# Kernel optimization log

Measured on AMD Instinct MI355X. Metric: run time of the kernel, lower is better.

The kernel has to match this reference:

```python
import jax, jax.numpy as jnp
import numpy as np

VOCAB = 32000
DIM = 1024
DEPTH = 4
SEQ = 512
HEADS = 16
NMB = 4
MAXMEM = NMB * SEQ  # 2048
RAMP = 128
COEF = 1e-06
B = 4
DH = DIM // HEADS


def _ln(x, g, b):
    mu = jnp.mean(x, axis=-1, keepdims=True)
    v = jnp.mean((x - mu) ** 2, axis=-1, keepdims=True)
    return (x - mu) / jnp.sqrt(v + 1e-5) * g + b


def setup_inputs() -> dict:
    key = jax.random.key(0)
    ks = jax.random.split(key, 24)
    s = 0.02
    inp = {
        'tokens': jax.random.randint(ks[0], (B, SEQ), 0, VOCAB),
        'mems': jax.random.normal(ks[1], (DEPTH, B, MAXMEM, DIM), jnp.float32) * s,
        'times': jax.random.randint(ks[2], (DEPTH, MAXMEM), 0, 4096, dtype=jnp.int32),
        'token_emb': jax.random.normal(ks[3], (VOCAB, DIM), jnp.float32) * s,
        'expire_W': jax.random.normal(ks[4], (DEPTH, DIM), jnp.float32) * s,
        'expire_b': jnp.full((DEPTH,), -float(MAXMEM), jnp.float32),  # torch init constant
        'ln1_g': jnp.ones((DEPTH, DIM), jnp.float32),
        'ln1_b': jnp.zeros((DEPTH, DIM), jnp.float32),
        'Wq': jax.random.normal(ks[5], (DEPTH, DIM, DIM), jnp.float32) * s,
        'Wkv': jax.random.normal(ks[6], (DEPTH, DIM, 2 * DIM), jnp.float32) * s,
        'Wo': jax.random.normal(ks[7], (DEPTH, DIM, DIM), jnp.float32) * s,
        'bo': jnp.zeros((DEPTH, DIM), jnp.float32),
        'ln2_g': jnp.ones((DEPTH, DIM), jnp.float32),
        'ln2_b': jnp.zeros((DEPTH, DIM), jnp.float32),
        'W1': jax.random.normal(ks[8], (DEPTH, DIM, 4 * DIM), jnp.float32) * s,
        'b1': jnp.zeros((DEPTH, 4 * DIM), jnp.float32),
        'W2': jax.random.normal(ks[9], (DEPTH, 4 * DIM, DIM), jnp.float32) * s,
        'b2': jnp.zeros((DEPTH, DIM), jnp.float32),
        'logits_W': jax.random.normal(ks[10], (DIM, VOCAB), jnp.float32) * s,
        'logits_b': jnp.zeros((VOCAB,), jnp.float32),
    }
    return inp


def reference(tokens, mems, times, token_emb, expire_W, expire_b, ln1_g, ln1_b,
              Wq, Wkv, Wo, bo, ln2_g, ln2_b, W1, b1, W2, b2, logits_W, logits_b):
    n, M = SEQ, MAXMEM
    scale = DH ** -0.5
    x = token_emb[tokens]  # (B, n, DIM)
    # causal mask over concat(mem, x): query i may attend key j iff j <= i + M
    causal = jnp.triu(jnp.ones((n, M + n), bool), k=M + 1)  # True = masked
    aux = jnp.float32(0.0)
    new_mems, new_times = [], []
    tnew = jnp.arange(n - 1, -1, -1, dtype=times.dtype)
    for d in range(DEPTH):
        mem = mems[d]                       # (B, M, DIM)
        t = times[d].astype(jnp.float32)    # (M,)
        hidden = x
        # --- expire span: per-memory-slot soft retention mask ---
        exps = jax.nn.sigmoid(mem @ expire_W[d] + expire_b[d]) * M  # (B, M)
        r = exps[:, None, None, :] - t[None, None, None, :]          # (B,1,1,M)
        r = jnp.pad(r, ((0, 0), (0, 0), (0, 0), (0, n)), constant_values=1.0)
        emask = jnp.clip(r / RAMP + 1.0, 0.0, 1.0)                   # (B,1,1,M+n)
        # --- pre-norm causal attention over concat(mem, x_normed) ---
        xn = _ln(x, ln1_g[d], ln1_b[d])
        q = (xn @ Wq[d]).reshape(B, n, HEADS, DH).transpose(0, 2, 1, 3)
        ctx = jnp.concatenate([mem, xn], axis=1)                     # (B, M+n, DIM)
        kv = ctx @ Wkv[d]
        k = kv[..., :DIM].reshape(B, M + n, HEADS, DH).transpose(0, 2, 1, 3)
        v = kv[..., DIM:].reshape(B, M + n, HEADS, DH).transpose(0, 2, 1, 3)
        dots = jnp.einsum('bhid,bhjd->bhij', q, k) * scale
        dots = jnp.where(causal, -jnp.inf, dots)
        attn = jax.nn.softmax(dots, axis=-1) * emask
        out = jnp.einsum('bhij,bhjd->bhid', attn, v)
        out = out.transpose(0, 2, 1, 3).reshape(B, n, DIM)
        x = out @ Wo[d] + bo[d] + x
        # --- pre-norm FFN ---
        xn2 = _ln(x, ln2_g[d], ln2_b[d])
        x = jax.nn.gelu(xn2 @ W1[d] + b1[d], approximate=False) @ W2[d] + b2[d] + x
        aux = aux + (exps / SEQ).sum() * COEF
        # --- memory bookkeeping (detached) ---
        new_mems.append(jax.lax.stop_gradient(
            jnp.concatenate([mem, hidden], axis=1)[:, -M:]))
        new_times.append(jnp.concatenate([times[d] + n, tnew])[-M:])
    logits = x @ logits_W + logits_b
    return (logits, jnp.stack(new_mems), jnp.stack(new_times), aux)
```

## Files before the change

### kernel.cpp

```cpp
#include <hip/hip_runtime.h>
#include <cmath>

#define DIMC   1024
#define SEQC   512
#define BC     4
#define MC     2048
#define CTXC   2560
#define HEADSC 16
#define DHC    64
#define VOCABC 32000

using short8 = __attribute__((ext_vector_type(8))) short;
using f32x4  = __attribute__((ext_vector_type(4))) float;
using u16x4  = __attribute__((ext_vector_type(4))) unsigned short;
using u16x8  = __attribute__((ext_vector_type(8))) unsigned short;

__device__ __forceinline__ unsigned short f2bf(float f) {
    unsigned u = __float_as_uint(f);
    unsigned r = (u + 0x7fffu + ((u >> 16) & 1u)) >> 16;
    return (unsigned short)r;
}

__device__ __forceinline__ void glds16(const unsigned short* g, char* l) {
    __builtin_amdgcn_global_load_lds(
        (const __attribute__((address_space(1))) void*)g,
        (__attribute__((address_space(3))) void*)l, 16, 0, 0);
}

__global__ __launch_bounds__(256) void embed_kernel(const int* __restrict__ tokens,
                                                    const float* __restrict__ emb,
                                                    float* __restrict__ x) {
    int row = blockIdx.x;
    int tok = tokens[row];
    const float4 v = *(const float4*)(emb + (size_t)tok * DIMC + threadIdx.x * 4);
    *(float4*)(x + (size_t)row * DIMC + threadIdx.x * 4) = v;
}

__global__ __launch_bounds__(256) void times_init_kernel(const int* __restrict__ times,
                                                         float* __restrict__ out_times,
                                                         float* __restrict__ aux) {
    int i = blockIdx.x * 256 + threadIdx.x;
    if (i == 0) aux[0] = 0.0f;
    if (i < 4 * MC) {
        int d = i >> 11, m = i & (MC - 1);
        out_times[i] = (m < MC - SEQC) ? (float)(times[d * MC + SEQC + m] + SEQC)
                                       : (float)(MC - 1 - m);
    }
}

#define PREP_MEM 8192
#define PREP_XC  10240
#define PREP_LN  12288
#define PREP_TOT 24576
__global__ __launch_bounds__(256) void prep_kernel(
    const float* __restrict__ mem_d, const float* __restrict__ x,
    const float* __restrict__ eW, const float* __restrict__ eb,
    float* __restrict__ exps, float* __restrict__ aux,
    unsigned short* __restrict__ mem_b, float* __restrict__ out_mems_d,
    const float* __restrict__ g1, const float* __restrict__ b1v,
    unsigned short* __restrict__ xn_b,
    const float* __restrict__ Wq, const float* __restrict__ Wkv,
    const float* __restrict__ Wo, const float* __restrict__ W1,
    const float* __restrict__ W2,
    unsigned short* __restrict__ wq_t, unsigned short* __restrict__ wkv_t,
    unsigned short* __restrict__ wo_t, unsigned short* __restrict__ w1_t,
    unsigned short* __restrict__ w2_t) {
    __shared__ float sh[1056];
    const int bid = blockIdx.x, tid = threadIdx.x;
    if (bid < PREP_MEM) {
        int row = bid;
        int m = row & 2047, b = row >> 11;
        const float4 v = *(const float4*)(mem_d + (size_t)row * DIMC + tid * 4);
        const float4 w = *(const float4*)(eW + tid * 4);
        float s = v.x * w.x + v.y * w.y + v.z * w.z + v.w * w.w;
        for (int off = 32; off; off >>= 1) s += __shfl_down(s, off, 64);
        int wid = tid >> 6, lane = tid & 63;
        if (lane == 0) sh[wid] = s;
        u16x4 o = { f2bf(v.x), f2bf(v.y), f2bf(v.z), f2bf(v.w) };
        *(u16x4*)(mem_b + (size_t)row * DIMC + tid * 4) = o;
        if (m >= SEQC)
            *(float4*)(out_mems_d + ((size_t)(b * MC + m - SEQC)) * DIMC + tid * 4) = v;
        __syncthreads();
        if (tid == 0) {
            float z = sh[0] + sh[1] + sh[2] + sh[3] + eb[0];
            float e = (float)MC / (1.0f + expf(-z));
            exps[row] = e;
            atomicAdd(aux, e * (1e-6f / (float)SEQC));
        }
    } else if (bid < PREP_XC) {
        int r = bid - PREP_MEM;
        int b = r >> 9, i = r & 511;
        const float4 v = *(const float4*)(x + (size_t)r * DIMC + tid * 4);
        *(float4*)(out_mems_d + ((size_t)(b * MC + MC - SEQC + i)) * DIMC + tid * 4) = v;
    } else if (bid < PREP_LN) {
        int row = bid - PREP_XC;
        const float4 v = *(const float4*)(x + (size_t)row * DIMC + tid * 4);
        float s = v.x + v.y + v.z + v.w;
        float q = v.x * v.x + v.y * v.y + v.z * v.z + v.w * v.w;
        for (int off = 32; off; off >>= 1) {
            s += __shfl_down(s, off, 64);
            q += __shfl_down(q, off, 64);
        }
        int wid = tid >> 6, lane = tid & 63;
        if (lane == 0) { sh[wid] = s; sh[4 + wid] = q; }
        __syncthreads();
        if (tid == 0) {
            float S = sh[0] + sh[1] + sh[2] + sh[3];
            float Q = sh[4] + sh[5] + sh[6] + sh[7];
            float mu = S / DIMC;
            float var = Q / DIMC - mu * mu;
            sh[8] = mu;
            sh[9] = rsqrtf(var + 1e-5f);
        }
        __syncthreads();
        float mu = sh[8], rstd = sh[9];
        const float4 gg = *(const float4*)(g1 + tid * 4);
        const float4 bb = *(const float4*)(b1v + tid * 4);
        u16x4 o = { f2bf((v.x - mu) * rstd * gg.x + bb.x),
                    f2bf((v.y - mu) * rstd * gg.y + bb.y),
                    f2bf((v.z - mu) * rstd * gg.z + bb.z),
                    f2bf((v.w - mu) * rstd * gg.w + bb.w) };
        *(u16x4*)(xn_b + (size_t)row * DIMC + tid * 4) = o;
    } else {
        int t = bid - PREP_LN;
        const float* W; unsigned short* Wt; int K, N, tx, ty;
        if (t < 1024)      { W = Wq;  Wt = wq_t;  K = 1024; N = 1024; tx = t & 31;  ty = t >> 5; }
        else if (t < 3072) { int u = t - 1024; W = Wkv; Wt = wkv_t; K = 1024; N = 2048; tx = u & 63;  ty = u >> 6; }
        else if (t < 4096) { int u = t - 3072; W = Wo;  Wt = wo_t;  K = 1024; N = 1024; tx = u & 31;  ty = u >> 5; }
        else if (t < 8192) { int u = t - 4096; W = W1;  Wt = w1_t;  K = 1024; N = 4096; tx = u & 127; ty = u >> 7; }
        else               { int u = t - 8192; W = W2;  Wt = w2_t;  K = 4096; N = 1024; tx = u & 31;  ty = u >> 5; }
        int n0 = tx * 32, k0 = ty * 32;
        int r = tid >> 3, c = (tid & 7) * 4;
        const float4 v = *(const float4*)(W + (size_t)(k0 + r) * N + n0 + c);
        sh[r * 33 + c] = v.x; sh[r * 33 + c + 1] = v.y;
        sh[r * 33 + c + 2] = v.z; sh[r * 33 + c + 3] = v.w;
        __syncthreads();
        u16x4 o = { f2bf(sh[(c + 0) * 33 + r]), f2bf(sh[(c + 1) * 33 + r]),
                    f2bf(sh[(c + 2) * 33 + r]), f2bf(sh[(c + 3) * 33 + r]) };
        *(u16x4*)(Wt + (size_t)(n0 + r) * K + k0 + c) = o;
    }
}

__global__ __launch_bounds__(64) void compact_kernel(
    const float* __restrict__ exps, const int* __restrict__ times_d,
    int* __restrict__ cidx, float* __restrict__ em_c, int* __restrict__ cnt) {
    int b = blockIdx.x, lane = threadIdx.x;
    int c = 0;
    for (int it = 0; it < 32; ++it) {
        int j = it * 64 + lane;
        float e = exps[b * MC + j];
        float rr = (e - (float)times_d[j]) * (1.0f / 128.0f) + 1.0f;
        float em = fminf(fmaxf(rr, 0.0f), 1.0f);
        unsigned long long mk = __ballot(em > 0.0f);
        int pos = c + __popcll(mk & ((1ull << lane) - 1ull));
        if (em > 0.0f) {
            cidx[b * 2048 + pos] = j;
            em_c[b * 2048 + pos] = em;
        }
        c += __popcll(mk);
    }
    int padded = (c + 63) & ~63;
    for (int p = c + lane; p < padded; p += 64) {
        cidx[b * 2048 + p] = 0;
        em_c[b * 2048 + p] = 0.0f;
    }
    if (lane == 0) cnt[b] = padded >> 6;
}

__global__ __launch_bounds__(256) void ln_kernel(const float* __restrict__ in,
                                                 const float* __restrict__ g,
                                                 const float* __restrict__ b,
                                                 unsigned short* __restrict__ outb) {
    int row = blockIdx.x;
    int tid = threadIdx.x;
    const float4 v = *(const float4*)(in + (size_t)row * DIMC + tid * 4);
    float s = v.x + v.y + v.z + v.w;
    float q = v.x * v.x + v.y * v.y + v.z * v.z + v.w * v.w;
    for (int off = 32; off; off >>= 1) {
        s += __shfl_down(s, off, 64);
        q += __shfl_down(q, off, 64);
    }
    __shared__ float ss[4], sq[4];
    int wid = tid >> 6, lane = tid & 63;
    if (lane == 0) { ss[wid] = s; sq[wid] = q; }
    __syncthreads();
    if (tid == 0) {
        float S = ss[0] + ss[1] + ss[2] + ss[3];
        float Q = sq[0] + sq[1] + sq[2] + sq[3];
        float mu = S / DIMC;
        float var = Q / DIMC - mu * mu;
        ss[0] = mu;
        sq[0] = rsqrtf(var + 1e-5f);
    }
    __syncthreads();
    float mu = ss[0], rstd = sq[0];
    const float4 gg = *(const float4*)(g + tid * 4);
    const float4 bb = *(const float4*)(b + tid * 4);
    u16x4 o = { f2bf((v.x - mu) * rstd * gg.x + bb.x),
                f2bf((v.y - mu) * rstd * gg.y + bb.y),
                f2bf((v.z - mu) * rstd * gg.z + bb.z),
                f2bf((v.w - mu) * rstd * gg.w + bb.w) };
    *(u16x4*)(outb + (size_t)row * DIMC + tid * 4) = o;
}

__global__ __launch_bounds__(256) void wt_kernel(const float* __restrict__ W,
                                                 unsigned short* __restrict__ Wt,
                                                 int K, int N) {
    __shared__ float t[32][33];
    int tid = threadIdx.x;
    int n0 = blockIdx.x * 32, k0 = blockIdx.y * 32;
    int r = tid >> 3, c = (tid & 7) * 4;
    const float4 v = *(const float4*)(W + (size_t)(k0 + r) * N + n0 + c);
    t[r][c] = v.x; t[r][c + 1] = v.y; t[r][c + 2] = v.z; t[r][c + 3] = v.w;
    __syncthreads();
    u16x4 o = { f2bf(t[c + 0][r]), f2bf(t[c + 1][r]),
                f2bf(t[c + 2][r]), f2bf(t[c + 3][r]) };
    *(u16x4*)(Wt + (size_t)(n0 + r) * K + k0 + c) = o;
}

__global__ __launch_bounds__(256) void vt_kernel(const unsigned short* __restrict__ kvb,
                                                 unsigned short* __restrict__ vT) {
    __shared__ unsigned short t[64][72];
    int jt = blockIdx.x, dt = blockIdx.y, b = blockIdx.z;
    int j0 = MC + jt * 64;
    int tid = threadIdx.x;
    int r = tid >> 3, c = (tid & 7) * 8;
    #pragma unroll
    for (int p = 0; p < 2; ++p) {
        u16x8 v = *(const u16x8*)(kvb + ((size_t)(b * CTXC + j0 + r + p * 32)) * 2048
                                  + 1024 + dt * 64 + c);
        *(u16x8*)&t[r + p * 32][c] = v;
    }
    __syncthreads();
    #pragma unroll
    for (int p = 0; p < 2; ++p) {
        int dr = r + p * 32;
        u16x8 o = { t[c + 0][dr], t[c + 1][dr], t[c + 2][dr], t[c + 3][dr],
                    t[c + 4][dr], t[c + 5][dr], t[c + 6][dr], t[c + 7][dr] };
        *(u16x8*)(vT + ((size_t)(b * 1024 + dt * 64 + dr)) * CTXC + j0 + c) = o;
    }
}

__global__ __launch_bounds__(256) void vtc_kernel(const unsigned short* __restrict__ kvb,
                                                  const int* __restrict__ cidx,
                                                  const int* __restrict__ cnt,
                                                  unsigned short* __restrict__ vTc) {
    int ct = blockIdx.x, dt = blockIdx.y, b = blockIdx.z;
    if (ct >= cnt[b]) return;
    __shared__ unsigned short t[64][72];
    int tid = threadIdx.x;
    int r = tid >> 3, c = (tid & 7) * 8;
    #pragma unroll
    for (int p = 0; p < 2; ++p) {
        int row = cidx[b * 2048 + ct * 64 + r + p * 32];
        u16x8 v = *(const u16x8*)(kvb + ((size_t)(b * CTXC + row)) * 2048
                                  + 1024 + dt * 64 + c);
        *(u16x8*)&t[r + p * 32][c] = v;
    }
    __syncthreads();
    #pragma unroll
    for (int p = 0; p < 2; ++p) {
        int dr = r + p * 32;
        u16x8 o = { t[c + 0][dr], t[c + 1][dr], t[c + 2][dr], t[c + 3][dr],
                    t[c + 4][dr], t[c + 5][dr], t[c + 6][dr], t[c + 7][dr] };
        *(u16x8*)(vTc + ((size_t)(b * 1024 + dt * 64 + dr)) * 2048 + ct * 64 + c) = o;
    }
}

template<bool GATHER, bool BIAS, bool GELU, bool RES, int RT>
__device__ __forceinline__ void gemm_body(
    unsigned short* As, unsigned short* Bs,
    const unsigned short* __restrict__ A, const unsigned short* __restrict__ A2,
    const unsigned short* __restrict__ Wt, const float* __restrict__ bias,
    const float* __restrict__ res, float* __restrict__ Cf,
    unsigned short* __restrict__ Cb, int K, int N, int bx, int by) {
    constexpr int MF = RT / 32;
    const int tid = threadIdx.x;
    const int lane = tid & 63, wave = tid >> 6;
    const int row0 = by * RT, col0 = bx * 128;

    const int seg = tid & 3;
    const int rr0 = tid >> 2;
    const unsigned short* arow[RT / 64];
    #pragma unroll
    for (int p = 0; p < RT / 64; ++p) {
        int r = row0 + p * 64 + rr0;
        if (GATHER) {
            int b = r / CTXC, rm = r - b * CTXC;
            arow[p] = (rm < MC) ? A + ((size_t)(b * MC + rm)) * K
                                : A2 + ((size_t)(b * SEQC + rm - MC)) * K;
        } else {
            arow[p] = A + (size_t)r * K;
        }
        arow[p] += seg * 8;
    }
    const unsigned short* brow[2];
    #pragma unroll
    for (int p = 0; p < 2; ++p)
        brow[p] = Wt + (size_t)(col0 + p * 64 + rr0) * K + seg * 8;

    char* lA0 = (char*)As + (size_t)(tid & 192) * 16;
    char* lB0 = (char*)Bs + (size_t)(tid & 192) * 16;
    char* lB1 = lB0 + 4096;

    f32x4 acc[MF][4] = {};

    const int wr = (wave >> 1) * (RT / 2), wc = (wave & 1) * 64;
    const int fr = lane & 15;
    const int k8 = (lane >> 4) * 8;
    const unsigned short* Ar = As + (size_t)(wr + fr) * 32 + k8;
    const unsigned short* Br = Bs + (size_t)(wc + fr) * 32 + k8;

    for (int k0 = 0; k0 < K; k0 += 32) {
        glds16(arow[0] + k0, lA0);
        if (RT == 128) glds16(arow[1] + k0, lA0 + 4096);
        glds16(brow[0] + k0, lB0);
        glds16(brow[1] + k0, lB1);
        __syncthreads();
        short8 a[MF], b[4];
        #pragma unroll
        for (int m = 0; m < MF; ++m) a[m] = *(const short8*)(Ar + m * 16 * 32);
        #pragma unroll
        for (int n = 0; n < 4; ++n) b[n] = *(const short8*)(Br + n * 16 * 32);
        #pragma unroll
        for (int m = 0; m < MF; ++m)
            #pragma unroll
            for (int n = 0; n < 4; ++n)
                acc[m][n] = __builtin_amdgcn_mfma_f32_16x16x32_bf16(a[m], b[n], acc[m][n], 0, 0, 0);
        __syncthreads();
    }

    const int orow = row0 + wr + (lane >> 4) * 4;
    const int ocol = col0 + wc + fr;
    #pragma unroll
    for (int n = 0; n < 4; ++n) {
        int c = ocol + n * 16;
        float bv = BIAS ? bias[c] : 0.0f;
        #pragma unroll
        for (int m = 0; m < MF; ++m) {
            #pragma unroll
            for (int i = 0; i < 4; ++i) {
                size_t idx = (size_t)(orow + m * 16 + i) * N + c;
                float v = acc[m][n][i] + bv;
                if (GELU) v = 0.5f * v * (1.0f + erff(v * 0.70710678118f));
                if (RES) v += res[idx];
                if (Cf) Cf[idx] = v;
                if (Cb) Cb[idx] = f2bf(v);
            }
        }
    }
}

__global__ __launch_bounds__(256) void qkv_gemm_kernel(
    const unsigned short* __restrict__ xn_b, const unsigned short* __restrict__ mem_b,
    const unsigned short* __restrict__ wq_t, const unsigned short* __restrict__ wkv_t,
    unsigned short* __restrict__ qb, unsigned short* __restrict__ kvb) {
    __shared__ unsigned short As[128 * 32];
    __shared__ unsigned short Bs[128 * 32];
    int id = blockIdx.x;
    if (id < 128) {
        gemm_body<false, false, false, false, 128>(As, Bs, xn_b, nullptr, wq_t,
            nullptr, nullptr, nullptr, qb, 1024, 1024, id & 7, id >> 3);
    } else {
        id -= 128;
        gemm_body<true, false, false, false, 128>(As, Bs, mem_b, xn_b, wkv_t,
            nullptr, nullptr, nullptr, kvb, 1024, 2048, id & 15, id >> 4);
    }
}

__global__ __launch_bounds__(256) void gemm64_kernel(
    const unsigned short* __restrict__ A, const unsigned short* __restrict__ Wt,
    const float* __restrict__ bias, const float* __restrict__ res,
    float* __restrict__ Cf, unsigned short* __restrict__ Cb, int K) {
    __shared__ unsigned short As[64 * 32];
    __shared__ unsigned short Bs[128 * 32];
    gemm_body<false, true, false, true, 64>(As, Bs, A, nullptr, Wt, bias, res,
        Cf, Cb, K, 1024, blockIdx.x, blockIdx.y);
}

__global__ __launch_bounds__(256) void ffn1_kernel(
    const unsigned short* __restrict__ A, const unsigned short* __restrict__ Wt,
    const float* __restrict__ bias, unsigned short* __restrict__ Cb) {
    __shared__ unsigned short As[128 * 32];
    __shared__ unsigned short Bs[128 * 32];
    gemm_body<false, true, true, false, 128>(As, Bs, A, nullptr, Wt, bias, nullptr,
        nullptr, Cb, 1024, 4096, blockIdx.x, blockIdx.y);
}

__global__ __launch_bounds__(256) void logits_kernel(
    const unsigned short* __restrict__ A, const unsigned short* __restrict__ Wt,
    const float* __restrict__ bias, float* __restrict__ Cf) {
    __shared__ unsigned short As[128 * 32];
    __shared__ unsigned short Bs[128 * 32];
    gemm_body<false, true, false, false, 128>(As, Bs, A, nullptr, Wt, bias, nullptr,
        Cf, nullptr, 1024, VOCABC, blockIdx.y, blockIdx.x);
}

__global__ __launch_bounds__(256) void attn_mfma_kernel(
    const unsigned short* __restrict__ qb,
    const unsigned short* __restrict__ kvb,
    const unsigned short* __restrict__ vT,
    const unsigned short* __restrict__ vTc,
    const int* __restrict__ cidx,
    const float* __restrict__ em_c,
    const int* __restrict__ cnt,
    unsigned short* __restrict__ outb) {
    __shared__ unsigned short K_s[64 * 64];
    __shared__ unsigned short V_s[64 * 64];
    __shared__ unsigned short p_s[4][16][72];
    __shared__ float em_s[64];
    const int tid = threadIdx.x;
    const int lane = tid & 63, wave = tid >> 6;
    const int qt = blockIdx.x, h = blockIdx.y, b = blockIdx.z;
    const int fr = lane & 15, g = lane >> 4;
    const int gq = qt * 64 + wave * 16;

    short8 aq[2];
    {
        const unsigned short* qp = qb + ((size_t)(b * SEQC + gq + fr)) * DIMC + h * DHC + g * 8;
        aq[0] = *(const short8*)qp;
        aq[1] = *(const short8*)(qp + 32);
    }

    const int sr = tid >> 3, ss = tid & 7;
    char* ldk = (char*)K_s + (tid & 192) * 16;
    char* ldv = (char*)V_s + (tid & 192) * 16;

    f32x4 acc_o[4] = {};
    float m_q = -1e30f, l_q = 0.0f;

    for (int kt = 0; kt < 32; ++kt) {
        const int jbase = kt * 64;
        __syncthreads();
        #pragma unroll
        for (int p = 0; p < 2; ++p) {
            int r = sr + p * 32, sw = (ss ^ (r & 7)) * 8;
            glds16(kvb + ((size_t)(b * CTXC + jbase + r)) * 2048 + h * DHC + sw, ldk + p * 4096);
        }
        __syncthreads();
        f32x4 sT[4] = {};
        #pragma unroll
        for (int ks = 0; ks < 2; ++ks)
            #pragma unroll
            for (int mf = 0; mf < 4; ++mf) {
                int row = mf * 16 + fr, sg = (ks * 4 + g) ^ (row & 7);
                short8 kk = *(const short8*)((const char*)K_s + row * 128 + sg * 16);
                sT[mf] = __builtin_amdgcn_mfma_f32_16x16x32_bf16(kk, aq[ks], sT[mf], 0, 0, 0);
            }
        float mx = sT[0][0];
        #pragma unroll
        for (int mf = 0; mf < 4; ++mf)
            #pragma unroll
            for (int i = 0; i < 4; ++i) mx = fmaxf(mx, sT[mf][i]);
        mx *= 0.125f;
        mx = fmaxf(mx, __shfl_xor(mx, 16, 64));
        mx = fmaxf(mx, __shfl_xor(mx, 32, 64));
        float mnew = fmaxf(m_q, mx);
        float fs = __expf(m_q - mnew);
        m_q = mnew;
        float ps = 0.0f;
        #pragma unroll
        for (int mf = 0; mf < 4; ++mf)
            #pragma unroll
            for (int i = 0; i < 4; ++i)
                ps += __expf(sT[mf][i] * 0.125f - mnew);
        ps += __shfl_xor(ps, 16, 64);
        ps += __shfl_xor(ps, 32, 64);
        l_q = l_q * fs + ps;
    }

    const int nlt = qt + 1;
    for (int lt = 0; lt < nlt; ++lt) {
        const int jbase = MC + lt * 64;
        __syncthreads();
        #pragma unroll
        for (int p = 0; p < 2; ++p) {
            int r = sr + p * 32, sw = (ss ^ (r & 7)) * 8;
            glds16(kvb + ((size_t)(b * CTXC + jbase + r)) * 2048 + h * DHC + sw, ldk + p * 4096);
            glds16(vT + ((size_t)(b * 1024 + h * DHC + r)) * CTXC + jbase + sw, ldv + p * 4096);
        }
        __syncthreads();
        f32x4 sT[4] = {};
        #pragma unroll
        for (int ks = 0; ks < 2; ++ks)
            #pragma unroll
            for (int mf = 0; mf < 4; ++mf) {
                int row = mf * 16 + fr, sg = (ks * 4 + g) ^ (row & 7);
                short8 kk = *(const short8*)((const char*)K_s + row * 128 + sg * 16);
                sT[mf] = __builtin_amdgcn_mfma_f32_16x16x32_bf16(kk, aq[ks], sT[mf], 0, 0, 0);
            }
        const int kq = gq + fr - lt * 64;
        float sv[4][4];
        #pragma unroll
        for (int mf = 0; mf < 4; ++mf)
            #pragma unroll
            for (int i = 0; i < 4; ++i) {
                int kl = mf * 16 + g * 4 + i;
                sv[mf][i] = (kl <= kq) ? sT[mf][i] * 0.125f : -1e30f;
            }
        float mx = sv[0][0];
        #pragma unroll
        for (int mf = 0; mf < 4; ++mf)
            #pragma unroll
            for (int i = 0; i < 4; ++i) mx = fmaxf(mx, sv[mf][i]);
        mx = fmaxf(mx, __shfl_xor(mx, 16, 64));
        mx = fmaxf(mx, __shfl_xor(mx, 32, 64));
        float mnew = fmaxf(m_q, mx);
        float fs = __expf(m_q - mnew);
        m_q = mnew;
        float ps = 0.0f;
        #pragma unroll
        for (int mf = 0; mf < 4; ++mf)
            #pragma unroll
            for (int i = 0; i < 4; ++i) {
                float pe = __expf(sv[mf][i] - mnew);
                ps += pe;
                p_s[wave][fr][mf * 16 + g * 4 + i] = f2bf(pe);
            }
        ps += __shfl_xor(ps, 16, 64);
        ps += __shfl_xor(ps, 32, 64);
        l_q = l_q * fs + ps;
        float fsr[4];
        #pragma unroll
        for (int i = 0; i < 4; ++i) fsr[i] = __shfl(fs, g * 4 + i, 64);
        #pragma unroll
        for (int n = 0; n < 4; ++n)
            #pragma unroll
            for (int i = 0; i < 4; ++i) acc_o[n][i] *= fsr[i];
        asm volatile("s_waitcnt lgkmcnt(0)" ::: "memory");
        #pragma unroll
        for (int ks = 0; ks < 2; ++ks) {
            short8 ap = *(const short8*)&p_s[wave][fr][ks * 32 + g * 8];
            #pragma unroll
            for (int n = 0; n < 4; ++n) {
                int row = n * 16 + fr, sg = (ks * 4 + g) ^ (row & 7);
                short8 bv = *(const short8*)((const char*)V_s + row * 128 + sg * 16);
                acc_o[n] = __builtin_amdgcn_mfma_f32_16x16x32_bf16(ap, bv, acc_o[n], 0, 0, 0);
            }
        }
    }

    const int nct = cnt[b];
    for (int ct = 0; ct < nct; ++ct) {
        __syncthreads();
        #pragma unroll
        for (int p = 0; p < 2; ++p) {
            int r = sr + p * 32, sw = (ss ^ (r & 7)) * 8;
            int row = cidx[b * 2048 + ct * 64 + r];
            glds16(kvb + ((size_t)(b * CTXC + row)) * 2048 + h * DHC + sw, ldk + p * 4096);
            glds16(vTc + ((size_t)(b * 1024 + h * DHC + r)) * 2048 + ct * 64 + sw, ldv + p * 4096);
        }
        if (tid < 64) em_s[tid] = em_c[b * 2048 + ct * 64 + tid];
        __syncthreads();
        f32x4 sT[4] = {};
        #pragma unroll
        for (int ks = 0; ks < 2; ++ks)
            #pragma unroll
            for (int mf = 0; mf < 4; ++mf) {
                int row = mf * 16 + fr, sg = (ks * 4 + g) ^ (row & 7);
                short8 kk = *(const short8*)((const char*)K_s + row * 128 + sg * 16);
                sT[mf] = __builtin_amdgcn_mfma_f32_16x16x32_bf16(kk, aq[ks], sT[mf], 0, 0, 0);
            }
        #pragma unroll
        for (int mf = 0; mf < 4; ++mf)
            #pragma unroll
            for (int i = 0; i < 4; ++i) {
                int key = mf * 16 + g * 4 + i;
                float pe = __expf(sT[mf][i] * 0.125f - m_q) * em_s[key];
                p_s[wave][fr][key] = f2bf(pe);
            }
        asm volatile("s_waitcnt lgkmcnt(0)" ::: "memory");
        #pragma unroll
        for (int ks = 0; ks < 2; ++ks) {
            short8 ap = *(const short8*)&p_s[wave][fr][ks * 32 + g * 8];
            #pragma unroll
            for (int n = 0; n < 4; ++n) {
                int row = n * 16 + fr, sg = (ks * 4 + g) ^ (row & 7);
                short8 bv = *(const short8*)((const char*)V_s + row * 128 + sg * 16);
                acc_o[n] = __builtin_amdgcn_mfma_f32_16x16x32_bf16(ap, bv, acc_o[n], 0, 0, 0);
            }
        }
    }

    float linv = 1.0f / l_q;
    float invr[4];
    #pragma unroll
    for (int i = 0; i < 4; ++i) invr[i] = __shfl(linv, g * 4 + i, 64);
    #pragma unroll
    for (int n = 0; n < 4; ++n) {
        #pragma unroll
        for (int i = 0; i < 4; ++i) {
            size_t idx = ((size_t)(b * SEQC + gq + g * 4 + i)) * DIMC + h * DHC + n * 16 + fr;
            outb[idx] = f2bf(acc_o[n][i] * invr[i]);
        }
    }
}

__global__ void aux_write_kernel(const float* __restrict__ aux, float* __restrict__ dst) {
    dst[0] = aux[0];
}

extern "C" void kernel_launch(void* const* d_in, const int* in_sizes, int n_in,
                              void* d_out, int out_size, void* d_ws, size_t ws_size,
                              hipStream_t stream) {
    const int*   tokens    = (const int*)d_in[0];
    const float* mems      = (const float*)d_in[1];
    const int*   times     = (const int*)d_in[2];
    const float* token_emb = (const float*)d_in[3];
    const float* expire_W  = (const float*)d_in[4];
    const float* expire_b  = (const float*)d_in[5];
    const float* ln1_g     = (const float*)d_in[6];
    const float* ln1_b     = (const float*)d_in[7];
    const float* Wq        = (const float*)d_in[8];
    const float* Wkv       = (const float*)d_in[9];
    const float* Wo        = (const float*)d_in[10];
    const float* bo        = (const float*)d_in[11];
    const float* ln2_g     = (const float*)d_in[12];
    const float* ln2_b     = (const float*)d_in[13];
    const float* W1        = (const float*)d_in[14];
    const float* b1        = (const float*)d_in[15];
    const float* W2        = (const float*)d_in[16];
    const float* b2        = (const float*)d_in[17];
    const float* logits_W  = (const float*)d_in[18];
    const float* logits_b  = (const float*)d_in[19];

    float* out = (float*)d_out;
    float* ws  = (float*)d_ws;

    float* x = ws;
    unsigned short* qb_b  = (unsigned short*)(ws + 2097152);
    unsigned short* kv_b  = (unsigned short*)(ws + 3145728);
    unsigned short* vT    = (unsigned short*)(ws + 13631488);
    unsigned short* xn_b  = (unsigned short*)(ws + 18874368);
    unsigned short* attn_b= (unsigned short*)(ws + 19922944);
    unsigned short* ffn_b = (unsigned short*)(ws + 20971520);
    unsigned short* mem_b = (unsigned short*)(ws + 25165824);
    unsigned short* x_b   = (unsigned short*)(ws + 29360128);
    unsigned short* wq_t  = (unsigned short*)(ws + 30408704);
    unsigned short* wkv_t = (unsigned short*)(ws + 30932992);
    unsigned short* wo_t  = (unsigned short*)(ws + 31981568);
    unsigned short* w1_t  = (unsigned short*)(ws + 32505856);
    unsigned short* w2_t  = (unsigned short*)(ws + 34603008);
    float* exps = ws + 36700160;
    float* aux  = ws + 36708352;
    unsigned short* vTc = (unsigned short*)(ws + 36708368);
    int*   cidx = (int*)(ws + 40902672);
    float* em_c = ws + 40910864;
    int*   cnt  = (int*)(ws + 40919056);
    unsigned short* lw_t = (unsigned short*)(ws + 2097152);

    float* out_logits = out;
    float* out_mems   = out + 65536000;
    float* out_times  = out + 99090432;

    embed_kernel<<<BC * SEQC, 256, 0, stream>>>(tokens, token_emb, x);
    times_init_kernel<<<32, 256, 0, stream>>>(times, out_times, aux);

    for (int d = 0; d < 4; ++d) {
        const float* mem_d = mems + (size_t)d * BC * MC * DIMC;
        prep_kernel<<<PREP_TOT, 256, 0, stream>>>(
            mem_d, x, expire_W + d * DIMC, expire_b + d, exps, aux,
            mem_b, out_mems + (size_t)d * BC * MC * DIMC,
            ln1_g + d * DIMC, ln1_b + d * DIMC, xn_b,
            Wq + (size_t)d * DIMC * DIMC, Wkv + (size_t)d * DIMC * 2 * DIMC,
            Wo + (size_t)d * DIMC * DIMC, W1 + (size_t)d * DIMC * 4 * DIMC,
            W2 + (size_t)d * 4 * DIMC * DIMC,
            wq_t, wkv_t, wo_t, w1_t, w2_t);
        compact_kernel<<<BC, 64, 0, stream>>>(exps, times + d * MC, cidx, em_c, cnt);
        qkv_gemm_kernel<<<1408, 256, 0, stream>>>(xn_b, mem_b, wq_t, wkv_t, qb_b, kv_b);
        vt_kernel<<<dim3(8, 16, BC), 256, 0, stream>>>(kv_b, vT);
        vtc_kernel<<<dim3(32, 16, BC), 256, 0, stream>>>(kv_b, cidx, cnt, vTc);
        attn_mfma_kernel<<<dim3(8, HEADSC, BC), 256, 0, stream>>>(
            qb_b, kv_b, vT, vTc, cidx, em_c, cnt, attn_b);
        gemm64_kernel<<<dim3(8, 32), 256, 0, stream>>>(
            attn_b, wo_t, bo + d * DIMC, x, x, nullptr, DIMC);
        ln_kernel<<<BC * SEQC, 256, 0, stream>>>(x, ln2_g + d * DIMC, ln2_b + d * DIMC, xn_b);
        ffn1_kernel<<<dim3(32, 16), 256, 0, stream>>>(xn_b, w1_t, b1 + d * 4 * DIMC, ffn_b);
        if (d < 3) {
            gemm64_kernel<<<dim3(8, 32), 256, 0, stream>>>(
                ffn_b, w2_t, b2 + d * DIMC, x, x, nullptr, 4 * DIMC);
        } else {
            gemm64_kernel<<<dim3(8, 32), 256, 0, stream>>>(
                ffn_b, w2_t, b2 + d * DIMC, x, nullptr, x_b, 4 * DIMC);
        }
    }

    wt_kernel<<<dim3(1000, 32), 256, 0, stream>>>(logits_W, lw_t, DIMC, VOCABC);
    logits_kernel<<<dim3(16, 250), 256, 0, stream>>>(x_b, lw_t, logits_b, out_logits);
    aux_write_kernel<<<1, 1, 0, stream>>>(aux, out + 99098624);
}
```

Measured before the change: 1.796 ms.

## Double-buffer LDS tiles in GEMM and attention to overlap loads with MFMA

Shared-memory tiles in the GEMM body and the attention kernel become two buffers. The next K-slice, or the next K/V tile, is issued via global_load_lds before computing on the current buffer, and one barrier per iteration replaces the previous pair. The attention kernel merges its memory-statistics loop and its causal-local loop into a single pipelined loop, so prefetching continues across the boundary between them. This doubles LDS per block, which may lower occupancy, and the overlap depends on the barrier's wait placement.

```diff
diff --git a/kernel.cpp b/kernel.cpp
--- a/kernel.cpp
+++ b/kernel.cpp
@@ -299,24 +299,31 @@
     for (int p = 0; p < 2; ++p)
         brow[p] = Wt + (size_t)(col0 + p * 64 + rr0) * K + seg * 8;
 
-    char* lA0 = (char*)As + (size_t)(tid & 192) * 16;
-    char* lB0 = (char*)Bs + (size_t)(tid & 192) * 16;
-    char* lB1 = lB0 + 4096;
+    char* lA = (char*)As + (tid & 192) * 16;
+    char* lB = (char*)Bs + (tid & 192) * 16;
+
+    auto stage = [&](int k0, int q) {
+        char* a = lA + q * (RT * 64);
+        glds16(arow[0] + k0, a);
+        if (RT == 128) glds16(arow[1] + k0, a + 4096);
+        char* bp = lB + q * 8192;
+        glds16(brow[0] + k0, bp);
+        glds16(brow[1] + k0, bp + 4096);
+    };
 
     f32x4 acc[MF][4] = {};
 
     const int wr = (wave >> 1) * (RT / 2), wc = (wave & 1) * 64;
     const int fr = lane & 15;
     const int k8 = (lane >> 4) * 8;
-    const unsigned short* Ar = As + (size_t)(wr + fr) * 32 + k8;
-    const unsigned short* Br = Bs + (size_t)(wc + fr) * 32 + k8;
-
+
+    stage(0, 0);
+    __syncthreads();
+    int cur = 0;
     for (int k0 = 0; k0 < K; k0 += 32) {
-        glds16(arow[0] + k0, lA0);
-        if (RT == 128) glds16(arow[1] + k0, lA0 + 4096);
-        glds16(brow[0] + k0, lB0);
-        glds16(brow[1] + k0, lB1);
-        __syncthreads();
+        if (k0 + 32 < K) stage(k0 + 32, cur ^ 1);
+        const unsigned short* Ar = As + cur * (RT * 32) + (size_t)(wr + fr) * 32 + k8;
+        const unsigned short* Br = Bs + cur * (128 * 32) + (size_t)(wc + fr) * 32 + k8;
         short8 a[MF], b[4];
         #pragma unroll
         for (int m = 0; m < MF; ++m) a[m] = *(const short8*)(Ar + m * 16 * 32);
@@ -328,6 +335,7 @@
             for (int n = 0; n < 4; ++n)
                 acc[m][n] = __builtin_amdgcn_mfma_f32_16x16x32_bf16(a[m], b[n], acc[m][n], 0, 0, 0);
         __syncthreads();
+        cur ^= 1;
     }
 
     const int orow = row0 + wr + (lane >> 4) * 4;
@@ -355,8 +363,8 @@
     const unsigned short* __restrict__ xn_b, const unsigned short* __restrict__ mem_b,
     const unsigned short* __restrict__ wq_t, const unsigned short* __restrict__ wkv_t,
     unsigned short* __restrict__ qb, unsigned short* __restrict__ kvb) {
-    __shared__ unsigned short As[128 * 32];
-    __shared__ unsigned short Bs[128 * 32];
+    __shared__ unsigned short As[2 * 128 * 32];
+    __shared__ unsigned short Bs[2 * 128 * 32];
     int id = blockIdx.x;
     if (id < 128) {
         gemm_body<false, false, false, false, 128>(As, Bs, xn_b, nullptr, wq_t,
@@ -372,8 +380,8 @@
     const unsigned short* __restrict__ A, const unsigned short* __restrict__ Wt,
     const float* __restrict__ bias, const float* __restrict__ res,
     float* __restrict__ Cf, unsigned short* __restrict__ Cb, int K) {
-    __shared__ unsigned short As[64 * 32];
-    __shared__ unsigned short Bs[128 * 32];
+    __shared__ unsigned short As[2 * 64 * 32];
+    __shared__ unsigned short Bs[2 * 128 * 32];
     gemm_body<false, true, false, true, 64>(As, Bs, A, nullptr, Wt, bias, res,
         Cf, Cb, K, 1024, blockIdx.x, blockIdx.y);
 }
@@ -381,8 +389,8 @@
 __global__ __launch_bounds__(256) void ffn1_kernel(
     const unsigned short* __restrict__ A, const unsigned short* __restrict__ Wt,
     const float* __restrict__ bias, unsigned short* __restrict__ Cb) {
-    __shared__ unsigned short As[128 * 32];
-    __shared__ unsigned short Bs[128 * 32];
+    __shared__ unsigned short As[2 * 128 * 32];
+    __shared__ unsigned short Bs[2 * 128 * 32];
     gemm_body<false, true, true, false, 128>(As, Bs, A, nullptr, Wt, bias, nullptr,
         nullptr, Cb, 1024, 4096, blockIdx.x, blockIdx.y);
 }
@@ -390,8 +398,8 @@
 __global__ __launch_bounds__(256) void logits_kernel(
     const unsigned short* __restrict__ A, const unsigned short* __restrict__ Wt,
     const float* __restrict__ bias, float* __restrict__ Cf) {
-    __shared__ unsigned short As[128 * 32];
-    __shared__ unsigned short Bs[128 * 32];
+    __shared__ unsigned short As[2 * 128 * 32];
+    __shared__ unsigned short Bs[2 * 128 * 32];
     gemm_body<false, true, false, false, 128>(As, Bs, A, nullptr, Wt, bias, nullptr,
         Cf, nullptr, 1024, VOCABC, blockIdx.y, blockIdx.x);
 }
@@ -405,8 +413,8 @@
     const float* __restrict__ em_c,
     const int* __restrict__ cnt,
     unsigned short* __restrict__ outb) {
-    __shared__ unsigned short K_s[64 * 64];
-    __shared__ unsigned short V_s[64 * 64];
+    __shared__ unsigned short K_s[2][64 * 64];
+    __shared__ unsigned short V_s[2][64 * 64];
     __shared__ unsigned short p_s[4][16][72];
     __shared__ float em_s[64];
     const int tid = threadIdx.x;
@@ -423,121 +431,117 @@
     }
 
     const int sr = tid >> 3, ss = tid & 7;
-    char* ldk = (char*)K_s + (tid & 192) * 16;
-    char* ldv = (char*)V_s + (tid & 192) * 16;
+    const int wbase = (tid & 192) * 16;
 
     f32x4 acc_o[4] = {};
     float m_q = -1e30f, l_q = 0.0f;
 
-    for (int kt = 0; kt < 32; ++kt) {
-        const int jbase = kt * 64;
-        __syncthreads();
+    const int nt = 33 + qt;
+
+    auto stage12 = [&](int t, int q) {
+        const int jbase = t * 64;
         #pragma unroll
         for (int p = 0; p < 2; ++p) {
             int r = sr + p * 32, sw = (ss ^ (r & 7)) * 8;
-            glds16(kvb + ((size_t)(b * CTXC + jbase + r)) * 2048 + h * DHC + sw, ldk + p * 4096);
-        }
-        __syncthreads();
+            glds16(kvb + ((size_t)(b * CTXC + jbase + r)) * 2048 + h * DHC + sw,
+                   (char*)K_s[q] + wbase + p * 4096);
+            if (t >= 32)
+                glds16(vT + ((size_t)(b * 1024 + h * DHC + r)) * CTXC + jbase + sw,
+                       (char*)V_s[q] + wbase + p * 4096);
+        }
+    };
+
+    stage12(0, 0);
+    __syncthreads();
+    int cur = 0;
+    for (int t = 0; t < nt; ++t) {
+        if (t + 1 < nt) stage12(t + 1, cur ^ 1);
+
         f32x4 sT[4] = {};
         #pragma unroll
         for (int ks = 0; ks < 2; ++ks)
             #pragma unroll
             for (int mf = 0; mf < 4; ++mf) {
                 int row = mf * 16 + fr, sg = (ks * 4 + g) ^ (row & 7);
-                short8 kk = *(const short8*)((const char*)K_s + row * 128 + sg * 16);
+                short8 kk = *(const short8*)((const char*)K_s[cur] + row * 128 + sg * 16);
                 sT[mf] = __builtin_amdgcn_mfma_f32_16x16x32_bf16(kk, aq[ks], sT[mf], 0, 0, 0);
             }
-        float mx = sT[0][0];
-        #pragma unroll
-        for (int mf = 0; mf < 4; ++mf)
-            #pragma unroll
-            for (int i = 0; i < 4; ++i) mx = fmaxf(mx, sT[mf][i]);
-        mx *= 0.125f;
-        mx = fmaxf(mx, __shfl_xor(mx, 16, 64));
-        mx = fmaxf(mx, __shfl_xor(mx, 32, 64));
-        float mnew = fmaxf(m_q, mx);
-        float fs = __expf(m_q - mnew);
-        m_q = mnew;
-        float ps = 0.0f;
-        #pragma unroll
-        for (int mf = 0; mf < 4; ++mf)
-            #pragma unroll
-            for (int i = 0; i < 4; ++i)
-                ps += __expf(sT[mf][i] * 0.125f - mnew);
-        ps += __shfl_xor(ps, 16, 64);
-        ps += __shfl_xor(ps, 32, 64);
-        l_q = l_q * fs + ps;
-    }
-
-    const int nlt = qt + 1;
-    for (int lt = 0; lt < nlt; ++lt) {
-        const int jbase = MC + lt * 64;
-        __syncthreads();
-        #pragma unroll
-        for (int p = 0; p < 2; ++p) {
-            int r = sr + p * 32, sw = (ss ^ (r & 7)) * 8;
-            glds16(kvb + ((size_t)(b * CTXC + jbase + r)) * 2048 + h * DHC + sw, ldk + p * 4096);
-            glds16(vT + ((size_t)(b * 1024 + h * DHC + r)) * CTXC + jbase + sw, ldv + p * 4096);
-        }
-        __syncthreads();
-        f32x4 sT[4] = {};
-        #pragma unroll
-        for (int ks = 0; ks < 2; ++ks)
-            #pragma unroll
-            for (int mf = 0; mf < 4; ++mf) {
-                int row = mf * 16 + fr, sg = (ks * 4 + g) ^ (row & 7);
-                short8 kk = *(const short8*)((const char*)K_s + row * 128 + sg * 16);
-                sT[mf] = __builtin_amdgcn_mfma_f32_16x16x32_bf16(kk, aq[ks], sT[mf], 0, 0, 0);
+
+        if (t < 32) {
+            float mx = sT[0][0];
+            #pragma unroll
+            for (int mf = 0; mf < 4; ++mf)
+                #pragma unroll
+                for (int i = 0; i < 4; ++i) mx = fmaxf(mx, sT[mf][i]);
+            mx *= 0.125f;
+            mx = fmaxf(mx, __shfl_xor(mx, 16, 64));
+            mx = fmaxf(mx, __shfl_xor(mx, 32, 64));
+            float mnew = fmaxf(m_q, mx);
+            float fs = __expf(m_q - mnew);
+            m_q = mnew;
+            float ps = 0.0f;
+            #pragma unroll
+            for (int mf = 0; mf < 4; ++mf)
+                #pragma unroll
+                for (int i = 0; i < 4; ++i)
+                    ps += __expf(sT[mf][i] * 0.125f - mnew);
+            ps += __shfl_xor(ps, 16, 64);
+            ps += __shfl_xor(ps, 32, 64);
+            l_q = l_q * fs + ps;
+        } else {
+            const int lt = t - 32;
+            const int kq = gq + fr - lt * 64;
+            float sv[4][4];
+            #pragma unroll
+            for (int mf = 0; mf < 4; ++mf)
+                #pragma unroll
+                for (int i = 0; i < 4; ++i) {
+                    int kl = mf * 16 + g * 4 + i;
+                    sv[mf][i] = (kl <= kq) ? sT[mf][i] * 0.125f : -1e30f;
+                }
+            float mx = sv[0][0];
+            #pragma unroll
+            for (int mf = 0; mf < 4; ++mf)
+                #pragma unroll
+                for (int i = 0; i < 4; ++i) mx = fmaxf(mx, sv[mf][i]);
+            mx = fmaxf(mx, __shfl_xor(mx, 16, 64));
+            mx = fmaxf(mx, __shfl_xor(mx, 32, 64));
+            float mnew = fmaxf(m_q, mx);
+            float fs = __expf(m_q - mnew);
+            m_q = mnew;
+            float ps = 0.0f;
+            #pragma unroll
+            for (int mf = 0; mf < 4; ++mf)
+                #pragma unroll
+                for (int i = 0; i < 4; ++i) {
+                    float pe = __expf(sv[mf][i] - mnew);
+                    ps += pe;
+                    p_s[wave][fr][mf * 16 + g * 4 + i] = f2bf(pe);
+                }
+            ps += __shfl_xor(ps, 16, 64);
+            ps += __shfl_xor(ps, 32, 64);
+            l_q = l_q * fs + ps;
+            float fsr[4];
+            #pragma unroll
+            for (int i = 0; i < 4; ++i) fsr[i] = __shfl(fs, g * 4 + i, 64);
+            #pragma unroll
+            for (int n = 0; n < 4; ++n)
+                #pragma unroll
+                for (int i = 0; i < 4; ++i) acc_o[n][i] *= fsr[i];
+            asm volatile("s_waitcnt lgkmcnt(0)" ::: "memory");
+            #pragma unroll
+            for (int ks = 0; ks < 2; ++ks) {
+                short8 ap = *(const short8*)&p_s[wave][fr][ks * 32 + g * 8];
+                #pragma unroll
+                for (int n = 0; n < 4; ++n) {
+                    int row = n * 16 + fr, sg = (ks * 4 + g) ^ (row & 7);
+                    short8 bv = *(const short8*)((const char*)V_s[cur] + row * 128 + sg * 16);
+                    acc_o[n] = __builtin_amdgcn_mfma_f32_16x16x32_bf16(ap, bv, acc_o[n], 0, 0, 0);
+                }
             }
-        const int kq = gq + fr - lt * 64;
-        float sv[4][4];
-        #pragma unroll
-        for (int mf = 0; mf < 4; ++mf)
-            #pragma unroll
-            for (int i = 0; i < 4; ++i) {
-                int kl = mf * 16 + g * 4 + i;
-                sv[mf][i] = (kl <= kq) ? sT[mf][i] * 0.125f : -1e30f;
-            }
-        float mx = sv[0][0];
-        #pragma unroll
-        for (int mf = 0; mf < 4; ++mf)
-            #pragma unroll
-            for (int i = 0; i < 4; ++i) mx = fmaxf(mx, sv[mf][i]);
-        mx = fmaxf(mx, __shfl_xor(mx, 16, 64));
-        mx = fmaxf(mx, __shfl_xor(mx, 32, 64));
-        float mnew = fmaxf(m_q, mx);
-        float fs = __expf(m_q - mnew);
-        m_q = mnew;
-        float ps = 0.0f;
-        #pragma unroll
-        for (int mf = 0; mf < 4; ++mf)
-            #pragma unroll
-            for (int i = 0; i < 4; ++i) {
-                float pe = __expf(sv[mf][i] - mnew);
-                ps += pe;
-                p_s[wave][fr][mf * 16 + g * 4 + i] = f2bf(pe);
-            }
-        ps += __shfl_xor(ps, 16, 64);
-        ps += __shfl_xor(ps, 32, 64);
-        l_q = l_q * fs + ps;
-        float fsr[4];
-        #pragma unroll
-        for (int i = 0; i < 4; ++i) fsr[i] = __shfl(fs, g * 4 + i, 64);
-        #pragma unroll
-        for (int n = 0; n < 4; ++n)
-            #pragma unroll
-            for (int i = 0; i < 4; ++i) acc_o[n][i] *= fsr[i];
-        asm volatile("s_waitcnt lgkmcnt(0)" ::: "memory");
-        #pragma unroll
-        for (int ks = 0; ks < 2; ++ks) {
-            short8 ap = *(const short8*)&p_s[wave][fr][ks * 32 + g * 8];
-            #pragma unroll
-            for (int n = 0; n < 4; ++n) {
-                int row = n * 16 + fr, sg = (ks * 4 + g) ^ (row & 7);
-                short8 bv = *(const short8*)((const char*)V_s + row * 128 + sg * 16);
-                acc_o[n] = __builtin_amdgcn_mfma_f32_16x16x32_bf16(ap, bv, acc_o[n], 0, 0, 0);
-            }
-        }
+        }
+        __syncthreads();
+        cur ^= 1;
     }
 
     const int nct = cnt[b];
@@ -547,8 +551,10 @@
         for (int p = 0; p < 2; ++p) {
             int r = sr + p * 32, sw = (ss ^ (r & 7)) * 8;
             int row = cidx[b * 2048 + ct * 64 + r];
-            glds16(kvb + ((size_t)(b * CTXC + row)) * 2048 + h * DHC + sw, ldk + p * 4096);
-            glds16(vTc + ((size_t)(b * 1024 + h * DHC + r)) * 2048 + ct * 64 + sw, ldv + p * 4096);
+            glds16(kvb + ((size_t)(b * CTXC + row)) * 2048 + h * DHC + sw,
+                   (char*)K_s[0] + wbase + p * 4096);
+            glds16(vTc + ((size_t)(b * 1024 + h * DHC + r)) * 2048 + ct * 64 + sw,
+                   (char*)V_s[0] + wbase + p * 4096);
         }
         if (tid < 64) em_s[tid] = em_c[b * 2048 + ct * 64 + tid];
         __syncthreads();
@@ -558,7 +564,7 @@
             #pragma unroll
             for (int mf = 0; mf < 4; ++mf) {
                 int row = mf * 16 + fr, sg = (ks * 4 + g) ^ (row & 7);
-                short8 kk = *(const short8*)((const char*)K_s + row * 128 + sg * 16);
+                short8 kk = *(const short8*)((const char*)K_s[0] + row * 128 + sg * 16);
                 sT[mf] = __builtin_amdgcn_mfma_f32_16x16x32_bf16(kk, aq[ks], sT[mf], 0, 0, 0);
             }
         #pragma unroll
@@ -576,7 +582,7 @@
             #pragma unroll
             for (int n = 0; n < 4; ++n) {
                 int row = n * 16 + fr, sg = (ks * 4 + g) ^ (row & 7);
-                short8 bv = *(const short8*)((const char*)V_s + row * 128 + sg * 16);
+                short8 bv = *(const short8*)((const char*)V_s[0] + row * 128 + sg * 16);
                 acc_o[n] = __builtin_amdgcn_mfma_f32_16x16x32_bf16(ap, bv, acc_o[n], 0, 0, 0);
             }
         }
```

Measured after the change: 1.838 ms. +2.4%, slower.
